# Kernel optimization log

Measured on AMD Instinct MI355X. Metric: run time of the kernel, lower is better.

Reference implementation:

```python
import jax, jax.numpy as jnp
import numpy as np
from jax import lax

NUM_HEADS = 8
N_WIN = 4
TOPK = 4


def setup_inputs() -> dict:
    key = jax.random.key(0)
    ks = jax.random.split(key, 5)
    B, C, H, W, D = 1, 128, 24, 24, 24
    x = jax.random.normal(ks[0], (B, C, H, W, D), dtype=jnp.float32)
    w_qkv = jax.random.normal(ks[1], (3 * C, C), dtype=jnp.float32) * 0.02
    b_qkv = jnp.zeros((3 * C,), dtype=jnp.float32)
    w_lepe = jax.random.normal(ks[2], (C, 1, 3, 3, 3), dtype=jnp.float32) * 0.05
    b_lepe = jnp.zeros((C,), dtype=jnp.float32)
    w_out = jax.random.normal(ks[3], (C, C), dtype=jnp.float32) * 0.02
    b_out = jnp.zeros((C,), dtype=jnp.float32)
    return {"x": x, "w_qkv": w_qkv, "b_qkv": b_qkv, "w_lepe": w_lepe,
            "b_lepe": b_lepe, "w_out": w_out, "b_out": b_out}


def reference(x, w_qkv, b_qkv, w_lepe, b_lepe, w_out, b_out):
    B, C, H, W, D = x.shape
    nh, nw, topk = NUM_HEADS, N_WIN, TOPK
    hd = C // nh
    rs = (H // nw, W // nw, D // nw)  # region size per axis
    nreg = nw ** 3
    scale = C ** (-0.5)

    # qkv projection (1x1 conv == channel matmul)
    qkv = jnp.einsum('bchwd,oc->bohwd', x, w_qkv) + b_qkv[None, :, None, None, None]
    q, k, v = jnp.split(qkv, 3, axis=1)

    # ---- region-level routing (detached in torch -> stop_gradient) ----
    def region_mean(t):  # (B,C,H,W,D) -> (B,C,nw,nw,nw)
        return t.reshape(B, C, nw, rs[0], nw, rs[1], nw, rs[2]).mean(axis=(3, 5, 7))
    q_r = region_mean(lax.stop_gradient(q)).transpose(0, 2, 3, 4, 1).reshape(B, nreg, C)
    k_r = region_mean(lax.stop_gradient(k)).reshape(B, C, nreg)
    a_r = jnp.einsum('bnc,bck->bnk', q_r, k_r)  # (B, nreg, nreg)
    _, idx = lax.top_k(a_r, topk)               # (B, nreg, topk)
    idx = jnp.broadcast_to(idx[:, None], (B, nh, nreg, topk))

    # ---- grid2seq: (B,C,H,W,D) -> (B,nh,nreg,reg_tokens,hd) ----
    def g2s(t):
        t = t.reshape(B, nh, hd, nw, rs[0], nw, rs[1], nw, rs[2])
        t = t.transpose(0, 1, 3, 5, 7, 4, 6, 8, 2)  # b m h w t p q u d
        return t.reshape(B, nh, nreg, rs[0] * rs[1] * rs[2], hd)
    qs, ks_, vs = g2s(q), g2s(k), g2s(v)

    # gather top-k kv regions per (batch, head, query-region)
    gather = jax.vmap(jax.vmap(lambda kv, i: kv[i]))  # over B and heads
    kg = gather(ks_, idx).reshape(B, nh, nreg, topk * rs[0] * rs[1] * rs[2], hd)
    vg = gather(vs, idx).reshape(B, nh, nreg, topk * rs[0] * rs[1] * rs[2], hd)

    attn = jax.nn.softmax(jnp.einsum('bmnqh,bmnkh->bmnqk', qs * scale, kg), axis=-1)
    o = jnp.einsum('bmnqk,bmnkh->bmnqh', attn, vg)

    # ---- seq2grid ----
    o = o.reshape(B, nh, nw, nw, nw, rs[0], rs[1], rs[2], hd)
    o = o.transpose(0, 1, 8, 2, 5, 3, 6, 4, 7).reshape(B, C, H, W, D)

    # lepe: depthwise 3x3x3 conv on v
    lepe = lax.conv_general_dilated(
        v, w_lepe, window_strides=(1, 1, 1), padding=[(1, 1)] * 3,
        dimension_numbers=('NCDHW', 'OIDHW', 'NCDHW'), feature_group_count=C)
    lepe = lepe + b_lepe[None, :, None, None, None]
    o = o + lepe

    out = jnp.einsum('bchwd,oc->bohwd', o, w_out) + b_out[None, :, None, None, None]
    return out
```

## Files before the change

kernel.cpp:

```cpp
#include <hip/hip_runtime.h>
#include <math.h>

#define S 13824
#define RT 216
#define SCALE 0.08838834764831845f

__global__ __launch_bounds__(256) void proj_kernel(
    const float* __restrict__ in, const float* __restrict__ w,
    const float* __restrict__ bias, float* __restrict__ outp, int OC) {
  __shared__ float xs[128][64];
  const int tid = threadIdx.x;
  const int sbase = blockIdx.x * 64;
  for (int i = tid; i < 128 * 64; i += 256)
    xs[i >> 6][i & 63] = in[(size_t)(i >> 6) * S + sbase + (i & 63)];
  __syncthreads();
  const int sl = tid & 63;
  const int wv = tid >> 6;
  const int ogN = OC >> 4;
  for (int og = 0; og < ogN; ++og) {
    const int o = og * 16 + wv * 4;
    const float4* w0 = (const float4*)(w + (size_t)o * 128);
    const float4* w1 = w0 + 32;
    const float4* w2 = w0 + 64;
    const float4* w3 = w0 + 96;
    float a0 = 0.f, a1 = 0.f, a2 = 0.f, a3 = 0.f;
#pragma unroll 8
    for (int c4 = 0; c4 < 32; ++c4) {
      float4 f0 = w0[c4], f1 = w1[c4], f2 = w2[c4], f3 = w3[c4];
      float x0 = xs[c4 * 4 + 0][sl], x1 = xs[c4 * 4 + 1][sl];
      float x2 = xs[c4 * 4 + 2][sl], x3 = xs[c4 * 4 + 3][sl];
      a0 += f0.x * x0 + f0.y * x1 + f0.z * x2 + f0.w * x3;
      a1 += f1.x * x0 + f1.y * x1 + f1.z * x2 + f1.w * x3;
      a2 += f2.x * x0 + f2.y * x1 + f2.z * x2 + f2.w * x3;
      a3 += f3.x * x0 + f3.y * x1 + f3.z * x2 + f3.w * x3;
    }
    size_t base = (size_t)o * S + sbase + sl;
    outp[base]         = a0 + bias[o + 0];
    outp[base + S]     = a1 + bias[o + 1];
    outp[base + 2 * S] = a2 + bias[o + 2];
    outp[base + 3 * S] = a3 + bias[o + 3];
  }
}

__global__ __launch_bounds__(256) void rmean_kernel(
    const float* __restrict__ qk, float* __restrict__ qr, float* __restrict__ kr) {
  const int n = blockIdx.x;
  const int tid = threadIdx.x, lane = tid & 63, wv = tid >> 6;
  const int rh = (n >> 4) * 6, rw = ((n >> 2) & 3) * 6, rd = (n & 3) * 6;
  int soff[4];
#pragma unroll
  for (int i = 0; i < 4; ++i) {
    int vx = lane + i * 64;
    if (vx < RT) {
      int p = vx / 36, qq = (vx / 6) % 6, u = vx % 6;
      soff[i] = (rh + p) * 576 + (rw + qq) * 24 + (rd + u);
    } else soff[i] = -1;
  }
  for (int ci = 0; ci < 64; ++ci) {
    int ch = wv + ci * 4;
    const float* src = qk + (size_t)ch * S;
    float ssum = 0.f;
#pragma unroll
    for (int i = 0; i < 4; ++i)
      if (soff[i] >= 0) ssum += src[soff[i]];
    for (int off = 32; off > 0; off >>= 1)
      ssum += __shfl_xor(ssum, off);
    if (lane == 0) {
      if (ch < 128) qr[n * 128 + ch] = ssum * (1.f / 216.f);
      else          kr[n * 128 + (ch - 128)] = ssum * (1.f / 216.f);
    }
  }
}

__global__ __launch_bounds__(64) void route_kernel(
    const float* __restrict__ qr, const float* __restrict__ kr, int* __restrict__ idxb) {
  const int n = blockIdx.x;
  const int t = threadIdx.x;
  float acc = 0.f;
  for (int c = 0; c < 128; ++c) acc += qr[n * 128 + c] * kr[t * 128 + c];
  float val = acc;
  int id = t;
  for (int j = 0; j < 4; ++j) {
    float bv = val;
    int bi = id;
    for (int off = 32; off > 0; off >>= 1) {
      float ov = __shfl_xor(bv, off);
      int oi = __shfl_xor(bi, off);
      if (ov > bv || (ov == bv && oi < bi)) { bv = ov; bi = oi; }
    }
    if (t == 0) idxb[n * 4 + j] = bi;
    if (id == bi) val = -INFINITY;
  }
}

__global__ __launch_bounds__(512, 4) void attn_kernel(
    const float* __restrict__ qkv, const int* __restrict__ idxb, float* __restrict__ go) {
  __shared__ __align__(16) float ks[2][RT][20];
  __shared__ __align__(16) float vs[2][RT][20];
  const float* q = qkv;
  const float* k = qkv + (size_t)128 * S;
  const float* v = qkv + (size_t)256 * S;
  const int n = blockIdx.x, mh = blockIdx.y;
  const int tid = threadIdx.x;
  const int h = tid >> 8;
  const int qi = tid & 255;
  const int rh = (n >> 4) * 6, rw = ((n >> 2) & 3) * 6, rd = (n & 3) * 6;
  const bool active = qi < RT;
  float ql[16];
  int sq = 0;
  if (active) {
    int p = qi / 36, qq = (qi / 6) % 6, u = qi % 6;
    sq = (rh + p) * 576 + (rw + qq) * 24 + (rd + u);
#pragma unroll
    for (int d = 0; d < 16; ++d)
      ql[d] = q[(size_t)(mh * 16 + d) * S + sq] * SCALE;
  }
  float m = -INFINITY, denom = 0.f;
  float o[16];
#pragma unroll
  for (int d = 0; d < 16; ++d) o[d] = 0.f;

  for (int j = 0; j < 2; ++j) {
    const int r = idxb[n * 4 + h * 2 + j];
    const int gh = (r >> 4) * 6, gw = ((r >> 2) & 3) * 6, gd = (r & 3) * 6;
    __syncthreads();
    for (int i = qi; i < RT * 16; i += 256) {
      int t = i % RT, d = i / RT;
      int p = t / 36, qq = (t / 6) % 6, u = t % 6;
      int s = (gh + p) * 576 + (gw + qq) * 24 + (gd + u);
      ks[h][t][d] = k[(size_t)(mh * 16 + d) * S + s];
      vs[h][t][d] = v[(size_t)(mh * 16 + d) * S + s];
    }
    __syncthreads();
    if (active) {
      for (int key0 = 0; key0 < RT; key0 += 4) {
        float dot[4];
#pragma unroll
        for (int kk = 0; kk < 4; ++kk) {
          const float4* kp = (const float4*)&ks[h][key0 + kk][0];
          float4 k0 = kp[0], k1 = kp[1], k2 = kp[2], k3 = kp[3];
          dot[kk] = ql[0] * k0.x + ql[1] * k0.y + ql[2] * k0.z + ql[3] * k0.w
                  + ql[4] * k1.x + ql[5] * k1.y + ql[6] * k1.z + ql[7] * k1.w
                  + ql[8] * k2.x + ql[9] * k2.y + ql[10] * k2.z + ql[11] * k2.w
                  + ql[12] * k3.x + ql[13] * k3.y + ql[14] * k3.z + ql[15] * k3.w;
        }
        float cmax = fmaxf(fmaxf(dot[0], dot[1]), fmaxf(dot[2], dot[3]));
        float mnew = fmaxf(m, cmax);
        float sc = __expf(m - mnew);
        m = mnew;
        denom *= sc;
#pragma unroll
        for (int d = 0; d < 16; ++d) o[d] *= sc;
#pragma unroll
        for (int kk = 0; kk < 4; ++kk) dot[kk] = __expf(dot[kk] - m);
#pragma unroll
        for (int kk = 0; kk < 4; ++kk) denom += dot[kk];
#pragma unroll
        for (int kk = 0; kk < 4; ++kk) {
          const float4* vp = (const float4*)&vs[h][key0 + kk][0];
          float4 v0 = vp[0], v1 = vp[1], v2 = vp[2], v3 = vp[3];
          float p = dot[kk];
          o[0] += p * v0.x;  o[1] += p * v0.y;  o[2] += p * v0.z;  o[3] += p * v0.w;
          o[4] += p * v1.x;  o[5] += p * v1.y;  o[6] += p * v1.z;  o[7] += p * v1.w;
          o[8] += p * v2.x;  o[9] += p * v2.y;  o[10] += p * v2.z; o[11] += p * v2.w;
          o[12] += p * v3.x; o[13] += p * v3.y; o[14] += p * v3.z; o[15] += p * v3.w;
        }
      }
    }
  }
  __syncthreads();
  float* mb = (float*)ks;
  if (h == 1 && active) {
    mb[qi * 18 + 0] = m;
    mb[qi * 18 + 1] = denom;
#pragma unroll
    for (int d = 0; d < 16; ++d) mb[qi * 18 + 2 + d] = o[d];
  }
  __syncthreads();
  if (h == 0 && active) {
    float m1 = mb[qi * 18 + 0], d1 = mb[qi * 18 + 1];
    float M = fmaxf(m, m1);
    float s0 = __expf(m - M), s1 = __expf(m1 - M);
    float inv = 1.f / (denom * s0 + d1 * s1);
#pragma unroll
    for (int d = 0; d < 16; ++d)
      go[(size_t)(mh * 16 + d) * S + sq] = (o[d] * s0 + mb[qi * 18 + 2 + d] * s1) * inv;
  }
}

__global__ __launch_bounds__(256) void lepe_kernel(
    const float* __restrict__ v, const float* __restrict__ wl,
    const float* __restrict__ bl, float* __restrict__ go) {
  const int c = blockIdx.y;
  const int s = blockIdx.x * 256 + threadIdx.x;
  const int h = s / 576, w = (s / 24) % 24, d = s % 24;
  const float* vp = v + (size_t)c * S;
  float wreg[27];
#pragma unroll
  for (int i = 0; i < 27; ++i) wreg[i] = wl[c * 27 + i];
  float acc = bl[c];
#pragma unroll
  for (int a = 0; a < 3; ++a) {
    int hh = h + a - 1;
    if (hh < 0 || hh >= 24) continue;
#pragma unroll
    for (int b = 0; b < 3; ++b) {
      int ww = w + b - 1;
      if (ww < 0 || ww >= 24) continue;
#pragma unroll
      for (int e = 0; e < 3; ++e) {
        int dd = d + e - 1;
        if (dd < 0 || dd >= 24) continue;
        acc += vp[hh * 576 + ww * 24 + dd] * wreg[a * 9 + b * 3 + e];
      }
    }
  }
  go[(size_t)c * S + s] += acc;
}

extern "C" void kernel_launch(void* const* d_in, const int* in_sizes, int n_in,
                              void* d_out, int out_size, void* d_ws, size_t ws_size,
                              hipStream_t stream) {
  const float* x      = (const float*)d_in[0];
  const float* w_qkv  = (const float*)d_in[1];
  const float* b_qkv  = (const float*)d_in[2];
  const float* w_lepe = (const float*)d_in[3];
  const float* b_lepe = (const float*)d_in[4];
  const float* w_out  = (const float*)d_in[5];
  const float* b_out  = (const float*)d_in[6];
  float* out = (float*)d_out;
  float* ws  = (float*)d_ws;

  float* qkv  = ws;
  float* go   = qkv + (size_t)384 * S;
  float* qr   = go + (size_t)128 * S;
  float* kr   = qr + 8192;
  int*   idxb = (int*)(kr + 8192);

  proj_kernel<<<216, 256, 0, stream>>>(x, w_qkv, b_qkv, qkv, 384);
  rmean_kernel<<<64, 256, 0, stream>>>(qkv, qr, kr);
  route_kernel<<<64, 64, 0, stream>>>(qr, kr, idxb);
  attn_kernel<<<dim3(64, 8), 512, 0, stream>>>(qkv, idxb, go);
  lepe_kernel<<<dim3(54, 128), 256, 0, stream>>>(qkv + (size_t)256 * S, w_lepe, b_lepe, go);
  proj_kernel<<<216, 256, 0, stream>>>(go, w_out, b_out, out, 128);
}
```

Before: 535.7 us.

## Split attention keys within a region across half-blocks and precompute gather offsets

```diff
diff --git a/kernel.cpp b/kernel.cpp
--- a/kernel.cpp
+++ b/kernel.cpp
@@ -93,19 +93,32 @@
   }
 }
 
-__global__ __launch_bounds__(512, 4) void attn_kernel(
+__global__ __launch_bounds__(512) void attn_kernel(
     const float* __restrict__ qkv, const int* __restrict__ idxb, float* __restrict__ go) {
-  __shared__ __align__(16) float ks[2][RT][20];
-  __shared__ __align__(16) float vs[2][RT][20];
+  __shared__ __align__(16) float ks[RT][20];
+  __shared__ __align__(16) float vs[RT][20];
   const float* q = qkv;
   const float* k = qkv + (size_t)128 * S;
   const float* v = qkv + (size_t)256 * S;
-  const int n = blockIdx.x, mh = blockIdx.y;
+  const int bid = blockIdx.x;
+  const int n = bid >> 3, mh = bid & 7;
   const int tid = threadIdx.x;
   const int h = tid >> 8;
   const int qi = tid & 255;
   const int rh = (n >> 4) * 6, rw = ((n >> 2) & 3) * 6, rd = (n & 3) * 6;
   const bool active = qi < RT;
+
+  int slot[7];
+#pragma unroll
+  for (int s2 = 0; s2 < 7; ++s2) {
+    int i = tid + 512 * s2;
+    if (i < RT * 16) {
+      int t = i % RT, d = i / RT;
+      int p = t / 36, qq = (t / 6) % 6, u = t % 6;
+      slot[s2] = (d << 20) | (t << 12) | (p * 576 + qq * 24 + u);
+    } else slot[s2] = -1;
+  }
+
   float ql[16];
   int sq = 0;
   if (active) {
@@ -120,51 +133,44 @@
 #pragma unroll
   for (int d = 0; d < 16; ++d) o[d] = 0.f;
 
-  for (int j = 0; j < 2; ++j) {
-    const int r = idxb[n * 4 + h * 2 + j];
-    const int gh = (r >> 4) * 6, gw = ((r >> 2) & 3) * 6, gd = (r & 3) * 6;
+  for (int j = 0; j < 4; ++j) {
+    const int r = idxb[n * 4 + j];
+    const int ghb = (r >> 4) * 3456 + ((r >> 2) & 3) * 144 + (r & 3) * 6;
     __syncthreads();
-    for (int i = qi; i < RT * 16; i += 256) {
-      int t = i % RT, d = i / RT;
-      int p = t / 36, qq = (t / 6) % 6, u = t % 6;
-      int s = (gh + p) * 576 + (gw + qq) * 24 + (gd + u);
-      ks[h][t][d] = k[(size_t)(mh * 16 + d) * S + s];
-      vs[h][t][d] = v[(size_t)(mh * 16 + d) * S + s];
+#pragma unroll
+    for (int s2 = 0; s2 < 7; ++s2) {
+      int sl = slot[s2];
+      if (sl >= 0) {
+        int d = sl >> 20, t = (sl >> 12) & 255, poff = sl & 4095;
+        size_t gidx = (size_t)(mh * 16 + d) * S + ghb + poff;
+        ks[t][d] = k[gidx];
+        vs[t][d] = v[gidx];
+      }
     }
     __syncthreads();
     if (active) {
-      for (int key0 = 0; key0 < RT; key0 += 4) {
-        float dot[4];
-#pragma unroll
-        for (int kk = 0; kk < 4; ++kk) {
-          const float4* kp = (const float4*)&ks[h][key0 + kk][0];
-          float4 k0 = kp[0], k1 = kp[1], k2 = kp[2], k3 = kp[3];
-          dot[kk] = ql[0] * k0.x + ql[1] * k0.y + ql[2] * k0.z + ql[3] * k0.w
+      for (int key = h * 108; key < h * 108 + 108; ++key) {
+        const float4* kp = (const float4*)&ks[key][0];
+        float4 k0 = kp[0], k1 = kp[1], k2 = kp[2], k3 = kp[3];
+        float dot = ql[0] * k0.x + ql[1] * k0.y + ql[2] * k0.z + ql[3] * k0.w
                   + ql[4] * k1.x + ql[5] * k1.y + ql[6] * k1.z + ql[7] * k1.w
                   + ql[8] * k2.x + ql[9] * k2.y + ql[10] * k2.z + ql[11] * k2.w
                   + ql[12] * k3.x + ql[13] * k3.y + ql[14] * k3.z + ql[15] * k3.w;
+        if (dot > m) {
+          float rsc = __expf(m - dot);
+          denom *= rsc;
+#pragma unroll
+          for (int d = 0; d < 16; ++d) o[d] *= rsc;
+          m = dot;
         }
-        float cmax = fmaxf(fmaxf(dot[0], dot[1]), fmaxf(dot[2], dot[3]));
-        float mnew = fmaxf(m, cmax);
-        float sc = __expf(m - mnew);
-        m = mnew;
-        denom *= sc;
-#pragma unroll
-        for (int d = 0; d < 16; ++d) o[d] *= sc;
-#pragma unroll
-        for (int kk = 0; kk < 4; ++kk) dot[kk] = __expf(dot[kk] - m);
-#pragma unroll
-        for (int kk = 0; kk < 4; ++kk) denom += dot[kk];
-#pragma unroll
-        for (int kk = 0; kk < 4; ++kk) {
-          const float4* vp = (const float4*)&vs[h][key0 + kk][0];
-          float4 v0 = vp[0], v1 = vp[1], v2 = vp[2], v3 = vp[3];
-          float p = dot[kk];
-          o[0] += p * v0.x;  o[1] += p * v0.y;  o[2] += p * v0.z;  o[3] += p * v0.w;
-          o[4] += p * v1.x;  o[5] += p * v1.y;  o[6] += p * v1.z;  o[7] += p * v1.w;
-          o[8] += p * v2.x;  o[9] += p * v2.y;  o[10] += p * v2.z; o[11] += p * v2.w;
-          o[12] += p * v3.x; o[13] += p * v3.y; o[14] += p * v3.z; o[15] += p * v3.w;
-        }
+        float p = __expf(dot - m);
+        denom += p;
+        const float4* vp = (const float4*)&vs[key][0];
+        float4 v0 = vp[0], v1 = vp[1], v2 = vp[2], v3 = vp[3];
+        o[0] += p * v0.x;  o[1] += p * v0.y;  o[2] += p * v0.z;  o[3] += p * v0.w;
+        o[4] += p * v1.x;  o[5] += p * v1.y;  o[6] += p * v1.z;  o[7] += p * v1.w;
+        o[8] += p * v2.x;  o[9] += p * v2.y;  o[10] += p * v2.z; o[11] += p * v2.w;
+        o[12] += p * v3.x; o[13] += p * v3.y; o[14] += p * v3.z; o[15] += p * v3.w;
       }
     }
   }
@@ -240,7 +246,7 @@
   proj_kernel<<<216, 256, 0, stream>>>(x, w_qkv, b_qkv, qkv, 384);
   rmean_kernel<<<64, 256, 0, stream>>>(qkv, qr, kr);
   route_kernel<<<64, 64, 0, stream>>>(qr, kr, idxb);
-  attn_kernel<<<dim3(64, 8), 512, 0, stream>>>(qkv, idxb, go);
+  attn_kernel<<<512, 512, 0, stream>>>(qkv, idxb, go);
   lepe_kernel<<<dim3(54, 128), 256, 0, stream>>>(qkv + (size_t)256 * S, w_lepe, b_lepe, go);
   proj_kernel<<<216, 256, 0, stream>>>(go, w_out, b_out, out, 128);
 }
```

After: 525.7 us. About the same (-1.9%).
